# Performance work log

Measured on AMD Instinct MI355X. Metric: run time of the kernel, lower is better.

Reference implementation:

```python
import jax, jax.numpy as jnp
import numpy as np

HEADS = 16  # matches init_kwargs


def setup_inputs() -> dict:
    key = jax.random.key(0)
    ks = jax.random.split(key, 9)
    N, L, E, D = 2, 2048, 1024, 64
    return {
        "query": jax.random.normal(ks[0], (N, L, E), dtype=jnp.float32),
        "keys": jax.random.normal(ks[1], (N, L, E), dtype=jnp.float32),
        "values": jax.random.normal(ks[2], (N, L, E), dtype=jnp.float32),
        "masks": jax.random.randint(ks[3], (N, 1, 1, L), 0, 2, dtype=jnp.int32),
        "Wq": jax.random.normal(ks[4], (D, D), dtype=jnp.float32) / np.sqrt(D),
        "Wk": jax.random.normal(ks[5], (D, D), dtype=jnp.float32) / np.sqrt(D),
        "Wv": jax.random.normal(ks[6], (D, D), dtype=jnp.float32) / np.sqrt(D),
        "Wo": jax.random.normal(ks[7], (E, E), dtype=jnp.float32) / np.sqrt(E),
        "bo": jax.random.normal(ks[8], (E,), dtype=jnp.float32),
    }


def reference(query, keys, values, masks, Wq, Wk, Wv, Wo, bo):
    N, Lq, E = query.shape
    Lk = keys.shape[1]
    H = HEADS
    D = E // H
    # split heads: [N, L, H, D]
    q = query.reshape(N, Lq, H, D)
    k = keys.reshape(N, Lk, H, D)
    v = values.reshape(N, Lk, H, D)
    # per-head linear projections (weights shared across heads); Linear: x @ W.T
    q = jnp.einsum("nqhd,ed->nqhe", q, Wq)
    k = jnp.einsum("nkhd,ed->nkhe", k, Wk)
    v = jnp.einsum("nkhd,ed->nkhe", v, Wv)
    # scores [N, H, Lq, Lk]
    scores = jnp.einsum("nqhd,nkhd->nhqk", q, k)
    scores = jnp.where(masks == 0, jnp.float32(-1e20), scores)
    # NOTE: original scales by sqrt(embed_size), not sqrt(head_dim)
    attn = jax.nn.softmax(scores / jnp.sqrt(jnp.float32(E)), axis=3)
    out = jnp.einsum("nhqk,nkhd->nqhd", attn, v).reshape(N, Lq, E)
    return out @ Wo.T + bo
```

## Files before the change

kernel.cpp:

```cpp
#include <hip/hip_runtime.h>


typedef __bf16 bf16_t;
typedef __bf16 bf16x4 __attribute__((ext_vector_type(4)));
typedef __bf16 bf16x8 __attribute__((ext_vector_type(8)));
typedef float f32x4 __attribute__((ext_vector_type(4)));
typedef unsigned int u32x4 __attribute__((ext_vector_type(4)));

#define MFMA16(a, b, c) __builtin_amdgcn_mfma_f32_16x16x32_bf16((a), (b), (c), 0, 0, 0)

#define GLOAD_LDS16(gp, lp)                                              \
    __builtin_amdgcn_global_load_lds(                                    \
        (const __attribute__((address_space(1))) void*)(gp),             \
        (__attribute__((address_space(3))) void*)(lp), 16, 0, 0)

__device__ inline bf16x8 cvt8(const float* __restrict__ p) {
    f32x4 a = *(const f32x4*)p;
    f32x4 b = *(const f32x4*)(p + 4);
    bf16x8 r;
    r[0] = (bf16_t)a[0]; r[1] = (bf16_t)a[1];
    r[2] = (bf16_t)a[2]; r[3] = (bf16_t)a[3];
    r[4] = (bf16_t)b[0]; r[5] = (bf16_t)b[1];
    r[6] = (bf16_t)b[2]; r[7] = (bf16_t)b[3];
    return r;
}

__device__ inline bf16x8 cvt8s(const f32x4 a, const f32x4 b) {
    bf16x8 r;
    r[0] = (bf16_t)a[0]; r[1] = (bf16_t)a[1];
    r[2] = (bf16_t)a[2]; r[3] = (bf16_t)a[3];
    r[4] = (bf16_t)b[0]; r[5] = (bf16_t)b[1];
    r[6] = (bf16_t)b[2]; r[7] = (bf16_t)b[3];
    return r;
}

__device__ inline float exp2_fast(float x) {
    float r;
    asm("v_exp_f32 %0, %1" : "=v"(r) : "v"(x));
    return r;
}

__device__ inline unsigned cvt_pk_bf16(float lo, float hi) {
    unsigned r;
    asm("v_cvt_pk_bf16_f32 %0, %1, %2" : "=v"(r) : "v"(lo), "v"(hi));
    return r;
}

__device__ inline void xchg_quads(unsigned &x, unsigned &y) {
    asm("v_permlane32_swap_b32 %0, %1\n\t"
        "v_permlane16_swap_b32 %0, %1"
        : "+v"(x), "+v"(y));
}

__global__ __launch_bounds__(256) void scan_kernel(
    const int* __restrict__ msk, int* __restrict__ excl, int* __restrict__ lmap,
    const float* __restrict__ Wq, const float* __restrict__ Wk,
    const float* __restrict__ Wv,
    bf16_t* __restrict__ Wqb, bf16_t* __restrict__ Wkb, bf16_t* __restrict__ Wvb)
{
    const int t = threadIdx.x;

    if (blockIdx.x >= 2) {
        const int wi = blockIdx.x - 2;
        const float* Ws = (wi == 0) ? Wq : (wi == 1) ? Wk : Wv;
        bf16_t* Wb = (wi == 0) ? Wqb : (wi == 1) ? Wkb : Wvb;
        const float scale = (wi == 0) ? 0.04508422f : 1.0f;
        #pragma unroll
        for (int j = 0; j < 4; j++) {
            int idx = t * 16 + j * 4;
            f32x4 v = *(const f32x4*)&Ws[idx];
            bf16x4 r;
            r[0] = (bf16_t)(v[0] * scale); r[1] = (bf16_t)(v[1] * scale);
            r[2] = (bf16_t)(v[2] * scale); r[3] = (bf16_t)(v[3] * scale);
            *(bf16x4*)&Wb[idx] = r;
        }
        return;
    }

    __shared__ int wsum[4];
    const int n = blockIdx.x;
    const int lane = t & 63, w = t >> 6;
    const int* m = msk + n * 2048;
    int* e = excl + n * 2049;
    int* lm = lmap + n * 2048;

    int v[8], s = 0;
    #pragma unroll
    for (int j = 0; j < 8; j++) { v[j] = (m[t * 8 + j] != 0); s += v[j]; }

    int inc = s;
    #pragma unroll
    for (int d = 1; d < 64; d <<= 1) {
        int o = __shfl_up(inc, d);
        if (lane >= d) inc += o;
    }
    if (lane == 63) wsum[w] = inc;
    __syncthreads();
    int off = 0;
    #pragma unroll
    for (int i = 0; i < 4; i++)
        if (i < w) off += wsum[i];

    int a = off + inc - s;
    #pragma unroll
    for (int j = 0; j < 8; j++) {
        e[t * 8 + j] = a;
        if (v[j]) lm[a] = t * 8 + j;
        a += v[j];
    }
    if (t == 255) e[2048] = a;
}

__global__ __launch_bounds__(256) void qkv_proj_kernel(
    const float* __restrict__ kin, const float* __restrict__ vin,
    const bf16_t* __restrict__ Wkb, const bf16_t* __restrict__ Wvb,
    const float* __restrict__ Wo,
    const int* __restrict__ excl, const int* __restrict__ lmap,
    bf16_t* __restrict__ kc, bf16_t* __restrict__ vcT, bf16_t* __restrict__ Wob)
{
    __shared__ __align__(16) char smem[51200];

    const int t = threadIdx.x;
    const int w = t >> 6, lane = t & 63, quad = lane >> 4, l16 = lane & 15;

    if (blockIdx.y == 2) {
        int idx = blockIdx.x * 1024 + t * 4;
        f32x4 v = *(const f32x4*)&Wo[idx];
        bf16x4 r;
        r[0] = (bf16_t)v[0]; r[1] = (bf16_t)v[1];
        r[2] = (bf16_t)v[2]; r[3] = (bf16_t)v[3];
        *(bf16x4*)&Wob[idx] = r;
        return;
    }

    if (blockIdx.y == 1) {
        bf16_t* Ct = (bf16_t*)smem;
        const int h = blockIdx.x & 15;
        const int ctile = blockIdx.x >> 4;
        const int n = ctile >> 5;
        const int c0 = (ctile & 31) * 64;
        const int Lc = excl[n * 2049 + 2048];
        if (c0 >= Lc) return;

        const int p0 = w * 16 + l16;
        int cs = c0 + p0; if (cs > Lc - 1) cs = Lc - 1;
        const int tg = lmap[n * 2048 + cs];
        const size_t rb = ((size_t)(n * 2048 + tg)) * 1024 + h * 64;

        bf16x8 b0 = cvt8(&vin[rb + quad * 8]);
        bf16x8 b1 = cvt8(&vin[rb + 32 + quad * 8]);

        #pragma unroll
        for (int nt = 0; nt < 4; nt++) {
            bf16x8 a0 = *(const bf16x8*)&Wvb[(nt * 16 + l16) * 64 + quad * 8];
            bf16x8 a1 = *(const bf16x8*)&Wvb[(nt * 16 + l16) * 64 + 32 + quad * 8];
            f32x4 acc = {0.f, 0.f, 0.f, 0.f};
            acc = MFMA16(a0, b0, acc);
            acc = MFMA16(a1, b1, acc);
            #pragma unroll
            for (int r = 0; r < 4; r++)
                Ct[(nt * 16 + quad * 4 + r) * 72 + w * 16 + l16] = (bf16_t)acc[r];
        }
        __syncthreads();
        const int cnt = (Lc - c0 < 64) ? (Lc - c0) : 64;
        const size_t ob2 = ((size_t)(n * 16 + h)) * 131072 + c0;
        #pragma unroll
        for (int pass = 0; pass < 2; pass++) {
            int r = pass * 32 + (t >> 3);
            int cb8 = (t & 7) * 8;
            if (cb8 < cnt) {
                if (cb8 + 8 <= cnt) {
                    *(bf16x8*)&vcT[ob2 + (size_t)r * 2048 + cb8] =
                        *(const bf16x8*)&Ct[r * 72 + cb8];
                } else {
                    for (int q = cb8; q < cnt; q++)
                        vcT[ob2 + (size_t)r * 2048 + q] = Ct[r * 72 + q];
                }
            }
        }
        return;
    }

    if (blockIdx.x >= 512) return;
    const int n = blockIdx.x >> 8;
    const int c0 = (blockIdx.x & 255) * 8;
    const int Lc = excl[n * 2049 + 2048];
    if (c0 >= Lc) return;

    float* Xs = (float*)smem;
    bf16_t* Ct2 = (bf16_t*)(smem + 32768);

    #pragma unroll
    for (int j = 0; j < 8; j++) {
        int br = w * 32 + j * 4;
        int srow = br + (lane >> 4);
        int scol = ((lane & 15) ^ (srow & 15)) * 4;
        int csx = c0 + (srow >> 4); if (csx > Lc - 1) csx = Lc - 1;
        int hs = srow & 15;
        int ls = lmap[n * 2048 + csx];
        GLOAD_LDS16(&kin[((size_t)((n * 2048 + ls) * 16 + hs)) * 64 + scol], &Xs[br * 64]);
    }
    __syncthreads();

    const int rbase = w * 32;
    bf16x8 a[2][2];
    #pragma unroll
    for (int qs = 0; qs < 2; qs++) {
        int row = rbase + qs * 16 + l16;
        const char* rowp = (const char*)Xs + (size_t)row * 256;
        int swb = (row & 15) << 4;
        #pragma unroll
        for (int c = 0; c < 2; c++) {
            f32x4 lo = *(const f32x4*)(rowp + ((c * 128 + quad * 32) ^ swb));
            f32x4 hi = *(const f32x4*)(rowp + ((c * 128 + quad * 32 + 16) ^ swb));
            a[qs][c] = cvt8s(lo, hi);
        }
    }

    f32x4 acc[4][2];
    #pragma unroll
    for (int nt = 0; nt < 4; nt++) {
        bf16x8 b0 = *(const bf16x8*)&Wkb[(nt * 16 + l16) * 64 + quad * 8];
        bf16x8 b1 = *(const bf16x8*)&Wkb[(nt * 16 + l16) * 64 + 32 + quad * 8];
        #pragma unroll
        for (int qs = 0; qs < 2; qs++) {
            f32x4 z = {0.f, 0.f, 0.f, 0.f};
            z = MFMA16(a[qs][0], b0, z);
            z = MFMA16(a[qs][1], b1, z);
            acc[nt][qs] = z;
        }
    }

    #pragma unroll
    for (int nt = 0; nt < 4; nt++)
        #pragma unroll
        for (int qs = 0; qs < 2; qs++)
            #pragma unroll
            for (int r = 0; r < 4; r++)
                Ct2[(rbase + qs * 16 + quad * 4 + r) * 72 + nt * 16 + l16] = (bf16_t)acc[nt][qs][r];
    __syncthreads();

    #pragma unroll
    for (int it = 0; it < 4; it++) {
        int j = it * 32 + (t >> 3);
        bf16x8 val = *(const bf16x8*)&Ct2[j * 72 + (t & 7) * 8];
        int c = c0 + (j >> 4), h2 = j & 15;
        if (c < Lc)
            *(bf16x8*)&kc[(((size_t)(n * 16 + h2)) * 2048 + c) * 64 + (t & 7) * 8] = val;
    }
}

__global__ __launch_bounds__(256) void attn_kernel(
    const float* __restrict__ qin, const bf16_t* __restrict__ Wqb,
    const bf16_t* __restrict__ kc, const bf16_t* __restrict__ vcT,
    const int* __restrict__ excl, bf16_t* __restrict__ ao)
{
    __shared__ __align__(16) char smem[65536];
    bf16_t* KtP = (bf16_t*)smem;
    bf16_t* VtP = (bf16_t*)(smem + 32768);
#define KT(buf, r, c) KtP[(buf) * 8192 + (r) * 64 + (c)]
#define VT(buf, r, c) VtP[(buf) * 8192 + (r) * 128 + (c)]

    const int t = threadIdx.x;
    const int w = t >> 6, lane = t & 63, quad = lane >> 4, l16 = lane & 15;

    const int flat = blockIdx.x;
    const int xcd = flat & 7, slot = flat >> 3;
    const int nh = xcd * 4 + (slot >> 4), qb = slot & 15;
    const int n = nh >> 4, h = nh & 15;
    const int qbase = qb * 128 + w * 32;
    const size_t nhbase = (size_t)nh * 131072;

    const int Lc = excl[n * 2049 + 2048];
    const int ntiles = (Lc + 127) >> 7;
    const int rbase = w * 32;

    bf16x8 aq[2][2];
    {
        float* Xq = (float*)smem;
        bf16_t* Qt = (bf16_t*)(smem + 32768);
        const int qrow0 = qb * 128;
        #pragma unroll
        for (int j = 0; j < 8; j++) {
            int br = w * 32 + j * 4;
            int srow = br + (lane >> 4);
            int scol = ((lane & 15) ^ (srow & 15)) * 4;
            GLOAD_LDS16(&qin[((size_t)(n * 2048 + qrow0 + srow)) * 1024 + h * 64 + scol],
                        &Xq[br * 64]);
        }
        __syncthreads();

        bf16x8 a[2][2];
        #pragma unroll
        for (int qs = 0; qs < 2; qs++) {
            int row = rbase + qs * 16 + l16;
            const char* rowp = (const char*)Xq + (size_t)row * 256;
            int swb = (row & 15) << 4;
            #pragma unroll
            for (int c = 0; c < 2; c++) {
                f32x4 lo = *(const f32x4*)(rowp + ((c * 128 + quad * 32) ^ swb));
                f32x4 hi = *(const f32x4*)(rowp + ((c * 128 + quad * 32 + 16) ^ swb));
                a[qs][c] = cvt8s(lo, hi);
            }
        }
        f32x4 pacc[4][2];
        #pragma unroll
        for (int nt = 0; nt < 4; nt++) {
            bf16x8 b0 = *(const bf16x8*)&Wqb[(nt * 16 + l16) * 64 + quad * 8];
            bf16x8 b1 = *(const bf16x8*)&Wqb[(nt * 16 + l16) * 64 + 32 + quad * 8];
            #pragma unroll
            for (int qs = 0; qs < 2; qs++) {
                f32x4 z = {0.f, 0.f, 0.f, 0.f};
                z = MFMA16(a[qs][0], b0, z);
                z = MFMA16(a[qs][1], b1, z);
                pacc[nt][qs] = z;
            }
        }
        #pragma unroll
        for (int nt = 0; nt < 4; nt++)
            #pragma unroll
            for (int qs = 0; qs < 2; qs++)
                #pragma unroll
                for (int r = 0; r < 4; r++) {
                    int row = rbase + qs * 16 + quad * 4 + r;
                    int col = nt * 16 + l16;
                    int byteoff = row * 128 + ((((col >> 3) ^ (row & 7)) << 4) | ((col & 7) << 1));
                    *(bf16_t*)((char*)Qt + byteoff) = (bf16_t)pacc[nt][qs][r];
                }
        #pragma unroll
        for (int qs = 0; qs < 2; qs++) {
            int row = rbase + qs * 16 + l16;
            #pragma unroll
            for (int c = 0; c < 2; c++)
                aq[qs][c] = *(const bf16x8*)((const char*)Qt + row * 128 +
                                             (((c * 4 + quad) ^ (row & 7)) << 4));
        }
        __syncthreads();
    }

    f32x4 o[2][4];
    float lsum[2] = {0.f, 0.f};
    #pragma unroll
    for (int qs = 0; qs < 2; qs++)
        #pragma unroll
        for (int dt = 0; dt < 4; dt++) {
            o[qs][dt][0] = 0.f; o[qs][dt][1] = 0.f; o[qs][dt][2] = 0.f; o[qs][dt][3] = 0.f;
        }

    const int ksrow = lane >> 3;
    const int kscol = ((lane & 7) ^ (lane >> 3)) * 8;
    const int swr = l16 & 7;
    const int ck0 = (quad ^ swr) * 8;
    const int ck1 = ((quad + 4) ^ swr) * 8;

#define STAGE_KV(buf, kn)                                                     \
    {                                                                         \
        _Pragma("unroll")                                                     \
        for (int j = 0; j < 4; j++) {                                         \
            int rb = w * 32 + j * 8;                                          \
            GLOAD_LDS16(&kc[nhbase + (size_t)((kn) + rb + ksrow) * 64 + kscol],\
                        &KT(buf, rb, 0));                                     \
        }                                                                     \
        _Pragma("unroll")                                                     \
        for (int j = 0; j < 4; j++) {                                         \
            int rb = w * 16 + j * 4;                                          \
            int d = rb + (lane >> 4);                                         \
            int sc = ((lane & 15) ^ (d & 15)) * 8;                            \
            GLOAD_LDS16(&vcT[nhbase + (size_t)d * 2048 + (kn) + sc],          \
                        &VT(buf, rb, 0));                                     \
        }                                                                     \
    }

    STAGE_KV(0, 0);

    for (int i = 0; i < ntiles; i++) {
        const int cb = i & 1, nb = cb ^ 1;
        const int k0 = i * 128;
        __syncthreads();

        if (i + 1 < ntiles) STAGE_KV(nb, k0 + 128);

        #pragma unroll
        for (int hf = 0; hf < 2; hf++) {
            const int kh = k0 + hf * 64;

            f32x4 st[2][4];
            __builtin_amdgcn_s_setprio(1);
            #pragma unroll
            for (int ct = 0; ct < 4; ct++) {
                bf16x8 kb0 = *(const bf16x8*)&KT(cb, hf * 64 + ct * 16 + l16, ck0);
                bf16x8 kb1 = *(const bf16x8*)&KT(cb, hf * 64 + ct * 16 + l16, ck1);
                #pragma unroll
                for (int qs = 0; qs < 2; qs++) {
                    f32x4 acc = {0.f, 0.f, 0.f, 0.f};
                    acc = MFMA16(kb0, aq[qs][0], acc);
                    acc = MFMA16(kb1, aq[qs][1], acc);
                    st[qs][ct] = acc;
                }
            }
            __builtin_amdgcn_s_setprio(0);

            if (kh + 64 <= Lc) {
                #pragma unroll
                for (int qs = 0; qs < 2; qs++)
                    #pragma unroll
                    for (int ct = 0; ct < 4; ct++)
                        #pragma unroll
                        for (int r = 0; r < 4; r++) {
                            float p = exp2_fast(st[qs][ct][r]);
                            lsum[qs] += p;
                            st[qs][ct][r] = p;
                        }
            } else {
                #pragma unroll
                for (int qs = 0; qs < 2; qs++)
                    #pragma unroll
                    for (int ct = 0; ct < 4; ct++)
                        #pragma unroll
                        for (int r = 0; r < 4; r++) {
                            int kk = kh + ct * 16 + quad * 4 + r;
                            float p = (kk < Lc) ? exp2_fast(st[qs][ct][r]) : 0.0f;
                            lsum[qs] += p;
                            st[qs][ct][r] = p;
                        }
            }

            bf16x8 bp[2][2];
            #pragma unroll
            for (int qs = 0; qs < 2; qs++) {
                unsigned u[4][2];
                #pragma unroll
                for (int ct = 0; ct < 4; ct++) {
                    u[ct][0] = cvt_pk_bf16(st[qs][ct][0], st[qs][ct][1]);
                    u[ct][1] = cvt_pk_bf16(st[qs][ct][2], st[qs][ct][3]);
                }
                #pragma unroll
                for (int hh = 0; hh < 2; hh++) {
                    unsigned b0 = u[2 * hh][0], b2 = u[2 * hh + 1][0];
                    xchg_quads(b0, b2);
                    unsigned b1 = u[2 * hh][1], b3 = u[2 * hh + 1][1];
                    xchg_quads(b1, b3);
                    u32x4 q4 = {b0, b1, b2, b3};
                    bp[qs][hh] = __builtin_bit_cast(bf16x8, q4);
                }
            }

            __builtin_amdgcn_s_setprio(1);
            #pragma unroll
            for (int dt = 0; dt < 4; dt++) {
                bf16x8 va0 = *(const bf16x8*)&VT(cb, dt * 16 + l16, ((hf * 8 + quad) ^ l16) * 8);
                bf16x8 va1 = *(const bf16x8*)&VT(cb, dt * 16 + l16, ((hf * 8 + 4 + quad) ^ l16) * 8);
                #pragma unroll
                for (int qs = 0; qs < 2; qs++) {
                    o[qs][dt] = MFMA16(va0, bp[qs][0], o[qs][dt]);
                    o[qs][dt] = MFMA16(va1, bp[qs][1], o[qs][dt]);
                }
            }
            __builtin_amdgcn_s_setprio(0);
        }
    }

    #pragma unroll
    for (int qs = 0; qs < 2; qs++) {
        float v = lsum[qs];
        v += __shfl_xor(v, 16);
        v += __shfl_xor(v, 32);
        float inv = 1.0f / v;
        const int q = qb * 128 + w * 32 + qs * 16 + l16;
        const size_t base = ((size_t)n * 2048 + q) * 1024 + h * 64;
        #pragma unroll
        for (int dt = 0; dt < 4; dt++) {
            bf16x4 ov;
            #pragma unroll
            for (int r = 0; r < 4; r++) ov[r] = (bf16_t)(o[qs][dt][r] * inv);
            *(bf16x4*)&ao[base + dt * 16 + quad * 4] = ov;
        }
    }
#undef KT
#undef VT
#undef STAGE_KV
}

__global__ __launch_bounds__(256, 2) void out_proj_kernel(
    const bf16_t* __restrict__ X, const bf16_t* __restrict__ Wob,
    const float* __restrict__ bo, float* __restrict__ out)
{
    __shared__ bf16_t Xs[2][128][64];
    __shared__ bf16_t Ws[2][128][64];

    const int t = threadIdx.x;
    const int w = t >> 6, lane = t & 63, quad = lane >> 4, l16 = lane & 15;
    const int Mbase = blockIdx.x * 128;
    const int Nbase = blockIdx.y * 128;
    const int mrow = (w & 1) * 64;
    const int ncol = (w >> 1) * 64;

    const int scol = ((lane & 7) ^ (lane >> 3)) * 8;
    const int swr  = l16 & 7;

    f32x4 acc[4][4];
    #pragma unroll
    for (int mi = 0; mi < 4; mi++)
        #pragma unroll
        for (int ni = 0; ni < 4; ni++) {
            acc[mi][ni][0] = 0.f; acc[mi][ni][1] = 0.f;
            acc[mi][ni][2] = 0.f; acc[mi][ni][3] = 0.f;
        }

    #pragma unroll
    for (int j = 0; j < 4; j++) {
        int br = w * 32 + j * 8;
        GLOAD_LDS16(&X[(size_t)(Mbase + br + (lane >> 3)) * 1024 + scol], &Xs[0][br][0]);
        GLOAD_LDS16(&Wob[(size_t)(Nbase + br + (lane >> 3)) * 1024 + scol], &Ws[0][br][0]);
    }

    for (int i = 0; i < 16; i++) {
        const int cb = i & 1, nb = cb ^ 1;
        __syncthreads();

        if (i < 15) {
            const int kn = (i + 1) * 64;
            #pragma unroll
            for (int j = 0; j < 4; j++) {
                int br = w * 32 + j * 8;
                GLOAD_LDS16(&X[(size_t)(Mbase + br + (lane >> 3)) * 1024 + kn + scol],
                            &Xs[nb][br][0]);
                GLOAD_LDS16(&Wob[(size_t)(Nbase + br + (lane >> 3)) * 1024 + kn + scol],
                            &Ws[nb][br][0]);
            }
        }

        #pragma unroll
        for (int c = 0; c < 2; c++) {
            bf16x8 bfr[4];
            #pragma unroll
            for (int ni = 0; ni < 4; ni++)
                bfr[ni] = *(const bf16x8*)&Ws[cb][ncol + ni * 16 + l16][((c * 4 + quad) ^ swr) * 8];
            #pragma unroll
            for (int mi = 0; mi < 4; mi++) {
                bf16x8 afr = *(const bf16x8*)&Xs[cb][mrow + mi * 16 + l16][((c * 4 + quad) ^ swr) * 8];
                #pragma unroll
                for (int ni = 0; ni < 4; ni++)
                    acc[mi][ni] = MFMA16(afr, bfr[ni], acc[mi][ni]);
            }
        }
    }

    #pragma unroll
    for (int ni = 0; ni < 4; ni++) {
        float b = bo[Nbase + ncol + ni * 16 + l16];
        #pragma unroll
        for (int mi = 0; mi < 4; mi++) {
            #pragma unroll
            for (int r = 0; r < 4; r++) {
                int row = Mbase + mrow + mi * 16 + quad * 4 + r;
                out[(size_t)row * 1024 + Nbase + ncol + ni * 16 + l16] = acc[mi][ni][r] + b;
            }
        }
    }
}

extern "C" void kernel_launch(void* const* d_in, const int* in_sizes, int n_in,
                              void* d_out, int out_size, void* d_ws, size_t ws_size,
                              hipStream_t stream)
{
    const float* qin = (const float*)d_in[0];
    const float* kin = (const float*)d_in[1];
    const float* vin = (const float*)d_in[2];
    const int*   msk = (const int*)d_in[3];
    const float* Wq  = (const float*)d_in[4];
    const float* Wk  = (const float*)d_in[5];
    const float* Wv  = (const float*)d_in[6];
    const float* Wo  = (const float*)d_in[7];
    const float* bo  = (const float*)d_in[8];
    float* out = (float*)d_out;

    bf16_t* ws  = (bf16_t*)d_ws;
    bf16_t* kc  = ws + 4194304;
    bf16_t* vcT = ws + 8388608;
    bf16_t* ao  = ws + 12582912;
    bf16_t* Wob = ws + 16777216;
    int* excl   = (int*)(ws + 17825792);
    int* lmap   = excl + 4100;
    bf16_t* Wqb = (bf16_t*)(lmap + 4096);
    bf16_t* Wkb = Wqb + 4096;
    bf16_t* Wvb = Wkb + 4096;

    scan_kernel<<<5, 256, 0, stream>>>(msk, excl, lmap, Wq, Wk, Wv, Wqb, Wkb, Wvb);
    qkv_proj_kernel<<<dim3(1024, 3), 256, 0, stream>>>(kin, vin, Wkb, Wvb, Wo,
                                                        excl, lmap, kc, vcT, Wob);
    attn_kernel<<<dim3(512), 256, 0, stream>>>(qin, Wqb, kc, vcT, excl, ao);
    out_proj_kernel<<<dim3(32, 8), 256, 0, stream>>>(ao, Wob, bo, out);
}
```

Measured before the change: 158.4 us.

## Split attention block across eight waves with sixteen query rows each

The attention kernel now launches 512 threads per block, so each of eight waves handles 16 query rows instead of 32, and K/V staging is spread across more threads. This raises the wave count per CU to hide latency of LDS reads and exp work. In exchange, each wave reuses each K/V LDS fragment for fewer MFMAs, so LDS read traffic per unit of compute doubles, and the larger block may limit how many blocks fit per CU.

```diff
diff --git a/kernel.cpp b/kernel.cpp
--- a/kernel.cpp
+++ b/kernel.cpp
@@ -250,7 +250,7 @@
     }
 }
 
-__global__ __launch_bounds__(256) void attn_kernel(
+__global__ __launch_bounds__(512) void attn_kernel(
     const float* __restrict__ qin, const bf16_t* __restrict__ Wqb,
     const bf16_t* __restrict__ kc, const bf16_t* __restrict__ vcT,
     const int* __restrict__ excl, bf16_t* __restrict__ ao)
@@ -268,21 +268,20 @@
     const int xcd = flat & 7, slot = flat >> 3;
     const int nh = xcd * 4 + (slot >> 4), qb = slot & 15;
     const int n = nh >> 4, h = nh & 15;
-    const int qbase = qb * 128 + w * 32;
     const size_t nhbase = (size_t)nh * 131072;
 
     const int Lc = excl[n * 2049 + 2048];
     const int ntiles = (Lc + 127) >> 7;
-    const int rbase = w * 32;
-
-    bf16x8 aq[2][2];
+    const int rbase = w * 16;
+
+    bf16x8 aq[2];
     {
         float* Xq = (float*)smem;
         bf16_t* Qt = (bf16_t*)(smem + 32768);
         const int qrow0 = qb * 128;
         #pragma unroll
-        for (int j = 0; j < 8; j++) {
-            int br = w * 32 + j * 4;
+        for (int j = 0; j < 4; j++) {
+            int br = w * 16 + j * 4;
             int srow = br + (lane >> 4);
             int scol = ((lane & 15) ^ (srow & 15)) * 4;
             GLOAD_LDS16(&qin[((size_t)(n * 2048 + qrow0 + srow)) * 1024 + h * 64 + scol],
@@ -290,62 +289,53 @@
         }
         __syncthreads();
 
-        bf16x8 a[2][2];
-        #pragma unroll
-        for (int qs = 0; qs < 2; qs++) {
-            int row = rbase + qs * 16 + l16;
+        bf16x8 a[2];
+        {
+            int row = rbase + l16;
             const char* rowp = (const char*)Xq + (size_t)row * 256;
             int swb = (row & 15) << 4;
             #pragma unroll
             for (int c = 0; c < 2; c++) {
                 f32x4 lo = *(const f32x4*)(rowp + ((c * 128 + quad * 32) ^ swb));
                 f32x4 hi = *(const f32x4*)(rowp + ((c * 128 + quad * 32 + 16) ^ swb));
-                a[qs][c] = cvt8s(lo, hi);
-            }
-        }
-        f32x4 pacc[4][2];
+                a[c] = cvt8s(lo, hi);
+            }
+        }
+        f32x4 pacc[4];
         #pragma unroll
         for (int nt = 0; nt < 4; nt++) {
             bf16x8 b0 = *(const bf16x8*)&Wqb[(nt * 16 + l16) * 64 + quad * 8];
             bf16x8 b1 = *(const bf16x8*)&Wqb[(nt * 16 + l16) * 64 + 32 + quad * 8];
-            #pragma unroll
-            for (int qs = 0; qs < 2; qs++) {
-                f32x4 z = {0.f, 0.f, 0.f, 0.f};
-                z = MFMA16(a[qs][0], b0, z);
-                z = MFMA16(a[qs][1], b1, z);
-                pacc[nt][qs] = z;
-            }
+            f32x4 z = {0.f, 0.f, 0.f, 0.f};
+            z = MFMA16(a[0], b0, z);
+            z = MFMA16(a[1], b1, z);
+            pacc[nt] = z;
         }
         #pragma unroll
         for (int nt = 0; nt < 4; nt++)
             #pragma unroll
-            for (int qs = 0; qs < 2; qs++)
-                #pragma unroll
-                for (int r = 0; r < 4; r++) {
-                    int row = rbase + qs * 16 + quad * 4 + r;
-                    int col = nt * 16 + l16;
-                    int byteoff = row * 128 + ((((col >> 3) ^ (row & 7)) << 4) | ((col & 7) << 1));
-                    *(bf16_t*)((char*)Qt + byteoff) = (bf16_t)pacc[nt][qs][r];
-                }
-        #pragma unroll
-        for (int qs = 0; qs < 2; qs++) {
-            int row = rbase + qs * 16 + l16;
+            for (int r = 0; r < 4; r++) {
+                int row = rbase + quad * 4 + r;
+                int col = nt * 16 + l16;
+                int byteoff = row * 128 + ((((col >> 3) ^ (row & 7)) << 4) | ((col & 7) << 1));
+                *(bf16_t*)((char*)Qt + byteoff) = (bf16_t)pacc[nt][r];
+            }
+        {
+            int row = rbase + l16;
             #pragma unroll
             for (int c = 0; c < 2; c++)
-                aq[qs][c] = *(const bf16x8*)((const char*)Qt + row * 128 +
-                                             (((c * 4 + quad) ^ (row & 7)) << 4));
+                aq[c] = *(const bf16x8*)((const char*)Qt + row * 128 +
+                                         (((c * 4 + quad) ^ (row & 7)) << 4));
         }
         __syncthreads();
     }
 
-    f32x4 o[2][4];
-    float lsum[2] = {0.f, 0.f};
-    #pragma unroll
-    for (int qs = 0; qs < 2; qs++)
-        #pragma unroll
-        for (int dt = 0; dt < 4; dt++) {
-            o[qs][dt][0] = 0.f; o[qs][dt][1] = 0.f; o[qs][dt][2] = 0.f; o[qs][dt][3] = 0.f;
-        }
+    f32x4 o[4];
+    float lsum = 0.f;
+    #pragma unroll
+    for (int dt = 0; dt < 4; dt++) {
+        o[dt][0] = 0.f; o[dt][1] = 0.f; o[dt][2] = 0.f; o[dt][3] = 0.f;
+    }
 
     const int ksrow = lane >> 3;
     const int kscol = ((lane & 7) ^ (lane >> 3)) * 8;
@@ -356,14 +346,14 @@
 #define STAGE_KV(buf, kn)                                                     \
     {                                                                         \
         _Pragma("unroll")                                                     \
-        for (int j = 0; j < 4; j++) {                                         \
-            int rb = w * 32 + j * 8;                                          \
+        for (int j = 0; j < 2; j++) {                                         \
+            int rb = w * 16 + j * 8;                                          \
             GLOAD_LDS16(&kc[nhbase + (size_t)((kn) + rb + ksrow) * 64 + kscol],\
                         &KT(buf, rb, 0));                                     \
         }                                                                     \
         _Pragma("unroll")                                                     \
-        for (int j = 0; j < 4; j++) {                                         \
-            int rb = w * 16 + j * 4;                                          \
+        for (int j = 0; j < 2; j++) {                                         \
+            int rb = w * 8 + j * 4;                                           \
             int d = rb + (lane >> 4);                                         \
             int sc = ((lane & 15) ^ (d & 15)) * 8;                            \
             GLOAD_LDS16(&vcT[nhbase + (size_t)d * 2048 + (kn) + sc],          \
@@ -384,55 +374,47 @@
         for (int hf = 0; hf < 2; hf++) {
             const int kh = k0 + hf * 64;
 
-            f32x4 st[2][4];
+            f32x4 st[4];
             __builtin_amdgcn_s_setprio(1);
             #pragma unroll
             for (int ct = 0; ct < 4; ct++) {
                 bf16x8 kb0 = *(const bf16x8*)&KT(cb, hf * 64 + ct * 16 + l16, ck0);
                 bf16x8 kb1 = *(const bf16x8*)&KT(cb, hf * 64 + ct * 16 + l16, ck1);
-                #pragma unroll
-                for (int qs = 0; qs < 2; qs++) {
-                    f32x4 acc = {0.f, 0.f, 0.f, 0.f};
-                    acc = MFMA16(kb0, aq[qs][0], acc);
-                    acc = MFMA16(kb1, aq[qs][1], acc);
-                    st[qs][ct] = acc;
-                }
+                f32x4 acc = {0.f, 0.f, 0.f, 0.f};
+                acc = MFMA16(kb0, aq[0], acc);
+                acc = MFMA16(kb1, aq[1], acc);
+                st[ct] = acc;
             }
             __builtin_amdgcn_s_setprio(0);
 
             if (kh + 64 <= Lc) {
                 #pragma unroll
-                for (int qs = 0; qs < 2; qs++)
+                for (int ct = 0; ct < 4; ct++)
                     #pragma unroll
-                    for (int ct = 0; ct < 4; ct++)
-                        #pragma unroll
-                        for (int r = 0; r < 4; r++) {
-                            float p = exp2_fast(st[qs][ct][r]);
-                            lsum[qs] += p;
-                            st[qs][ct][r] = p;
-                        }
+                    for (int r = 0; r < 4; r++) {
+                        float p = exp2_fast(st[ct][r]);
+                        lsum += p;
+                        st[ct][r] = p;
+                    }
             } else {
                 #pragma unroll
-                for (int qs = 0; qs < 2; qs++)
+                for (int ct = 0; ct < 4; ct++)
                     #pragma unroll
-                    for (int ct = 0; ct < 4; ct++)
-                        #pragma unroll
-                        for (int r = 0; r < 4; r++) {
-                            int kk = kh + ct * 16 + quad * 4 + r;
-                            float p = (kk < Lc) ? exp2_fast(st[qs][ct][r]) : 0.0f;
-                            lsum[qs] += p;
-                            st[qs][ct][r] = p;
-                        }
-            }
-
-            bf16x8 bp[2][2];
-            #pragma unroll
-            for (int qs = 0; qs < 2; qs++) {
+                    for (int r = 0; r < 4; r++) {
+                        int kk = kh + ct * 16 + quad * 4 + r;
+                        float p = (kk < Lc) ? exp2_fast(st[ct][r]) : 0.0f;
+                        lsum += p;
+                        st[ct][r] = p;
+                    }
+            }
+
+            bf16x8 bp[2];
+            {
                 unsigned u[4][2];
                 #pragma unroll
                 for (int ct = 0; ct < 4; ct++) {
-                    u[ct][0] = cvt_pk_bf16(st[qs][ct][0], st[qs][ct][1]);
-                    u[ct][1] = cvt_pk_bf16(st[qs][ct][2], st[qs][ct][3]);
+                    u[ct][0] = cvt_pk_bf16(st[ct][0], st[ct][1]);
+                    u[ct][1] = cvt_pk_bf16(st[ct][2], st[ct][3]);
                 }
                 #pragma unroll
                 for (int hh = 0; hh < 2; hh++) {
@@ -441,7 +423,7 @@
                     unsigned b1 = u[2 * hh][1], b3 = u[2 * hh + 1][1];
                     xchg_quads(b1, b3);
                     u32x4 q4 = {b0, b1, b2, b3};
-                    bp[qs][hh] = __builtin_bit_cast(bf16x8, q4);
+                    bp[hh] = __builtin_bit_cast(bf16x8, q4);
                 }
             }
 
@@ -450,29 +432,25 @@
             for (int dt = 0; dt < 4; dt++) {
                 bf16x8 va0 = *(const bf16x8*)&VT(cb, dt * 16 + l16, ((hf * 8 + quad) ^ l16) * 8);
                 bf16x8 va1 = *(const bf16x8*)&VT(cb, dt * 16 + l16, ((hf * 8 + 4 + quad) ^ l16) * 8);
-                #pragma unroll
-                for (int qs = 0; qs < 2; qs++) {
-                    o[qs][dt] = MFMA16(va0, bp[qs][0], o[qs][dt]);
-                    o[qs][dt] = MFMA16(va1, bp[qs][1], o[qs][dt]);
-                }
+                o[dt] = MFMA16(va0, bp[0], o[dt]);
+                o[dt] = MFMA16(va1, bp[1], o[dt]);
             }
             __builtin_amdgcn_s_setprio(0);
         }
     }
 
-    #pragma unroll
-    for (int qs = 0; qs < 2; qs++) {
-        float v = lsum[qs];
+    {
+        float v = lsum;
         v += __shfl_xor(v, 16);
         v += __shfl_xor(v, 32);
         float inv = 1.0f / v;
-        const int q = qb * 128 + w * 32 + qs * 16 + l16;
+        const int q = qb * 128 + w * 16 + l16;
         const size_t base = ((size_t)n * 2048 + q) * 1024 + h * 64;
         #pragma unroll
         for (int dt = 0; dt < 4; dt++) {
             bf16x4 ov;
             #pragma unroll
-            for (int r = 0; r < 4; r++) ov[r] = (bf16_t)(o[qs][dt][r] * inv);
+            for (int r = 0; r < 4; r++) ov[r] = (bf16_t)(o[dt][r] * inv);
             *(bf16x4*)&ao[base + dt * 16 + quad * 4] = ov;
         }
     }
@@ -589,6 +567,6 @@
     scan_kernel<<<5, 256, 0, stream>>>(msk, excl, lmap, Wq, Wk, Wv, Wqb, Wkb, Wvb);
     qkv_proj_kernel<<<dim3(1024, 3), 256, 0, stream>>>(kin, vin, Wkb, Wvb, Wo,
                                                         excl, lmap, kc, vcT, Wob);
-    attn_kernel<<<dim3(512), 256, 0, stream>>>(qin, Wqb, kc, vcT, excl, ao);
+    attn_kernel<<<dim3(512), 512, 0, stream>>>(qin, Wqb, kc, vcT, excl, ao);
     out_proj_kernel<<<dim3(32, 8), 256, 0, stream>>>(ao, Wob, bo, out);
 }
```

Measured after the change: 156.2 us. About the same (-1.4%).

## Split attention over key range with combine kernel; shrink out-proj N tile

Applied to the files above, without the earlier changes.

Splits each (batch, head, query-block) attention work item into two halves of the compacted key range, doubling the attention grid to 1024 blocks. Each half writes unnormalized fp32 partial outputs and row sums, and a new combine kernel adds them and normalizes into bf16. The key tile shrinks to 64 with smaller LDS, and the output projection uses 64-wide N tiles to double its grid. This raises occupancy and fills more CUs, but adds an extra launch and an fp32 round trip through global memory.

```diff
diff --git a/kernel.cpp b/kernel.cpp
--- a/kernel.cpp
+++ b/kernel.cpp
@@ -253,32 +253,37 @@
 __global__ __launch_bounds__(256) void attn_kernel(
     const float* __restrict__ qin, const bf16_t* __restrict__ Wqb,
     const bf16_t* __restrict__ kc, const bf16_t* __restrict__ vcT,
-    const int* __restrict__ excl, bf16_t* __restrict__ ao)
+    const int* __restrict__ excl, float* __restrict__ po, float* __restrict__ ls)
 {
-    __shared__ __align__(16) char smem[65536];
+    __shared__ __align__(16) char smem[32768];
     bf16_t* KtP = (bf16_t*)smem;
-    bf16_t* VtP = (bf16_t*)(smem + 32768);
-#define KT(buf, r, c) KtP[(buf) * 8192 + (r) * 64 + (c)]
-#define VT(buf, r, c) VtP[(buf) * 8192 + (r) * 128 + (c)]
+    bf16_t* VtP = (bf16_t*)(smem + 16384);
+#define KT(buf, r, c) KtP[(buf) * 4096 + (r) * 64 + (c)]
+#define VT(buf, r, c) VtP[(buf) * 4096 + (r) * 64 + (c)]
 
     const int t = threadIdx.x;
     const int w = t >> 6, lane = t & 63, quad = lane >> 4, l16 = lane & 15;
 
     const int flat = blockIdx.x;
     const int xcd = flat & 7, slot = flat >> 3;
-    const int nh = xcd * 4 + (slot >> 4), qb = slot & 15;
+    const int nh = xcd * 4 + (slot >> 5);
+    const int qb = (slot >> 1) & 15;
+    const int s  = slot & 1;
     const int n = nh >> 4, h = nh & 15;
-    const int qbase = qb * 128 + w * 32;
     const size_t nhbase = (size_t)nh * 131072;
 
     const int Lc = excl[n * 2049 + 2048];
-    const int ntiles = (Lc + 127) >> 7;
+    const int ntot  = (Lc + 63) >> 6;
+    const int nhalf = (ntot + 1) >> 1;
+    const int tile0 = s ? nhalf : 0;
+    const int tile1 = s ? ntot : nhalf;
     const int rbase = w * 32;
+    const int qbase = qb * 128 + rbase;
 
     bf16x8 aq[2][2];
     {
         float* Xq = (float*)smem;
-        bf16_t* Qt = (bf16_t*)(smem + 32768);
+        bf16_t* Qt = (bf16_t*)(smem + 16384);
         const int qrow0 = qb * 128;
         #pragma unroll
         for (int j = 0; j < 8; j++) {
@@ -303,6 +308,8 @@
                 a[qs][c] = cvt8s(lo, hi);
             }
         }
+        __syncthreads();
+
         f32x4 pacc[4][2];
         #pragma unroll
         for (int nt = 0; nt < 4; nt++) {
@@ -327,6 +334,7 @@
                     int byteoff = row * 128 + ((((col >> 3) ^ (row & 7)) << 4) | ((col & 7) << 1));
                     *(bf16_t*)((char*)Qt + byteoff) = (bf16_t)pacc[nt][qs][r];
                 }
+        __syncthreads();
         #pragma unroll
         for (int qs = 0; qs < 2; qs++) {
             int row = rbase + qs * 16 + l16;
@@ -356,108 +364,97 @@
 #define STAGE_KV(buf, kn)                                                     \
     {                                                                         \
         _Pragma("unroll")                                                     \
-        for (int j = 0; j < 4; j++) {                                         \
-            int rb = w * 32 + j * 8;                                          \
+        for (int j = 0; j < 2; j++) {                                         \
+            int rb = w * 16 + j * 8;                                          \
             GLOAD_LDS16(&kc[nhbase + (size_t)((kn) + rb + ksrow) * 64 + kscol],\
                         &KT(buf, rb, 0));                                     \
-        }                                                                     \
-        _Pragma("unroll")                                                     \
-        for (int j = 0; j < 4; j++) {                                         \
-            int rb = w * 16 + j * 4;                                          \
-            int d = rb + (lane >> 4);                                         \
-            int sc = ((lane & 15) ^ (d & 15)) * 8;                            \
-            GLOAD_LDS16(&vcT[nhbase + (size_t)d * 2048 + (kn) + sc],          \
+            GLOAD_LDS16(&vcT[nhbase + (size_t)(rb + ksrow) * 2048 + (kn) + kscol],\
                         &VT(buf, rb, 0));                                     \
         }                                                                     \
     }
 
-    STAGE_KV(0, 0);
-
-    for (int i = 0; i < ntiles; i++) {
-        const int cb = i & 1, nb = cb ^ 1;
-        const int k0 = i * 128;
+    if (tile0 < tile1) STAGE_KV(0, tile0 * 64);
+
+    for (int i = tile0; i < tile1; i++) {
+        const int cb = (i - tile0) & 1, nb = cb ^ 1;
+        const int k0 = i * 64;
         __syncthreads();
 
-        if (i + 1 < ntiles) STAGE_KV(nb, k0 + 128);
-
-        #pragma unroll
-        for (int hf = 0; hf < 2; hf++) {
-            const int kh = k0 + hf * 64;
-
-            f32x4 st[2][4];
-            __builtin_amdgcn_s_setprio(1);
+        if (i + 1 < tile1) STAGE_KV(nb, k0 + 64);
+
+        f32x4 st[2][4];
+        __builtin_amdgcn_s_setprio(1);
+        #pragma unroll
+        for (int ct = 0; ct < 4; ct++) {
+            bf16x8 kb0 = *(const bf16x8*)&KT(cb, ct * 16 + l16, ck0);
+            bf16x8 kb1 = *(const bf16x8*)&KT(cb, ct * 16 + l16, ck1);
+            #pragma unroll
+            for (int qs = 0; qs < 2; qs++) {
+                f32x4 acc = {0.f, 0.f, 0.f, 0.f};
+                acc = MFMA16(kb0, aq[qs][0], acc);
+                acc = MFMA16(kb1, aq[qs][1], acc);
+                st[qs][ct] = acc;
+            }
+        }
+        __builtin_amdgcn_s_setprio(0);
+
+        if (k0 + 64 <= Lc) {
+            #pragma unroll
+            for (int qs = 0; qs < 2; qs++)
+                #pragma unroll
+                for (int ct = 0; ct < 4; ct++)
+                    #pragma unroll
+                    for (int r = 0; r < 4; r++) {
+                        float p = exp2_fast(st[qs][ct][r]);
+                        lsum[qs] += p;
+                        st[qs][ct][r] = p;
+                    }
+        } else {
+            #pragma unroll
+            for (int qs = 0; qs < 2; qs++)
+                #pragma unroll
+                for (int ct = 0; ct < 4; ct++)
+                    #pragma unroll
+                    for (int r = 0; r < 4; r++) {
+                        int kk = k0 + ct * 16 + quad * 4 + r;
+                        float p = (kk < Lc) ? exp2_fast(st[qs][ct][r]) : 0.0f;
+                        lsum[qs] += p;
+                        st[qs][ct][r] = p;
+                    }
+        }
+
+        bf16x8 bp[2][2];
+        #pragma unroll
+        for (int qs = 0; qs < 2; qs++) {
+            unsigned u[4][2];
             #pragma unroll
             for (int ct = 0; ct < 4; ct++) {
-                bf16x8 kb0 = *(const bf16x8*)&KT(cb, hf * 64 + ct * 16 + l16, ck0);
-                bf16x8 kb1 = *(const bf16x8*)&KT(cb, hf * 64 + ct * 16 + l16, ck1);
-                #pragma unroll
-                for (int qs = 0; qs < 2; qs++) {
-                    f32x4 acc = {0.f, 0.f, 0.f, 0.f};
-                    acc = MFMA16(kb0, aq[qs][0], acc);
-                    acc = MFMA16(kb1, aq[qs][1], acc);
-                    st[qs][ct] = acc;
-                }
-            }
-            __builtin_amdgcn_s_setprio(0);
-
-            if (kh + 64 <= Lc) {
-                #pragma unroll
-                for (int qs = 0; qs < 2; qs++)
-                    #pragma unroll
-                    for (int ct = 0; ct < 4; ct++)
-                        #pragma unroll
-                        for (int r = 0; r < 4; r++) {
-                            float p = exp2_fast(st[qs][ct][r]);
-                            lsum[qs] += p;
-                            st[qs][ct][r] = p;
-                        }
-            } else {
-                #pragma unroll
-                for (int qs = 0; qs < 2; qs++)
-                    #pragma unroll
-                    for (int ct = 0; ct < 4; ct++)
-                        #pragma unroll
-                        for (int r = 0; r < 4; r++) {
-                            int kk = kh + ct * 16 + quad * 4 + r;
-                            float p = (kk < Lc) ? exp2_fast(st[qs][ct][r]) : 0.0f;
-                            lsum[qs] += p;
-                            st[qs][ct][r] = p;
-                        }
-            }
-
-            bf16x8 bp[2][2];
+                u[ct][0] = cvt_pk_bf16(st[qs][ct][0], st[qs][ct][1]);
+                u[ct][1] = cvt_pk_bf16(st[qs][ct][2], st[qs][ct][3]);
+            }
+            #pragma unroll
+            for (int hh = 0; hh < 2; hh++) {
+                unsigned b0 = u[2 * hh][0], b2 = u[2 * hh + 1][0];
+                xchg_quads(b0, b2);
+                unsigned b1 = u[2 * hh][1], b3 = u[2 * hh + 1][1];
+                xchg_quads(b1, b3);
+                u32x4 q4 = {b0, b1, b2, b3};
+                bp[qs][hh] = __builtin_bit_cast(bf16x8, q4);
+            }
+        }
+
+        __builtin_amdgcn_s_setprio(1);
+        #pragma unroll
+        for (int dt = 0; dt < 4; dt++) {
+            bf16x8 va0 = *(const bf16x8*)&VT(cb, dt * 16 + l16, ck0);
+            bf16x8 va1 = *(const bf16x8*)&VT(cb, dt * 16 + l16, ck1);
             #pragma unroll
             for (int qs = 0; qs < 2; qs++) {
-                unsigned u[4][2];
-                #pragma unroll
-                for (int ct = 0; ct < 4; ct++) {
-                    u[ct][0] = cvt_pk_bf16(st[qs][ct][0], st[qs][ct][1]);
-                    u[ct][1] = cvt_pk_bf16(st[qs][ct][2], st[qs][ct][3]);
-                }
-                #pragma unroll
-                for (int hh = 0; hh < 2; hh++) {
-                    unsigned b0 = u[2 * hh][0], b2 = u[2 * hh + 1][0];
-                    xchg_quads(b0, b2);
-                    unsigned b1 = u[2 * hh][1], b3 = u[2 * hh + 1][1];
-                    xchg_quads(b1, b3);
-                    u32x4 q4 = {b0, b1, b2, b3};
-                    bp[qs][hh] = __builtin_bit_cast(bf16x8, q4);
-                }
-            }
-
-            __builtin_amdgcn_s_setprio(1);
-            #pragma unroll
-            for (int dt = 0; dt < 4; dt++) {
-                bf16x8 va0 = *(const bf16x8*)&VT(cb, dt * 16 + l16, ((hf * 8 + quad) ^ l16) * 8);
-                bf16x8 va1 = *(const bf16x8*)&VT(cb, dt * 16 + l16, ((hf * 8 + 4 + quad) ^ l16) * 8);
-                #pragma unroll
-                for (int qs = 0; qs < 2; qs++) {
-                    o[qs][dt] = MFMA16(va0, bp[qs][0], o[qs][dt]);
-                    o[qs][dt] = MFMA16(va1, bp[qs][1], o[qs][dt]);
-                }
-            }
-            __builtin_amdgcn_s_setprio(0);
-        }
+                o[qs][dt] = MFMA16(va0, bp[qs][0], o[qs][dt]);
+                o[qs][dt] = MFMA16(va1, bp[qs][1], o[qs][dt]);
+            }
+        }
+        __builtin_amdgcn_s_setprio(0);
     }
 
     #pragma unroll
@@ -465,20 +462,50 @@
         float v = lsum[qs];
         v += __shfl_xor(v, 16);
         v += __shfl_xor(v, 32);
-        float inv = 1.0f / v;
-        const int q = qb * 128 + w * 32 + qs * 16 + l16;
-        const size_t base = ((size_t)n * 2048 + q) * 1024 + h * 64;
-        #pragma unroll
-        for (int dt = 0; dt < 4; dt++) {
-            bf16x4 ov;
-            #pragma unroll
-            for (int r = 0; r < 4; r++) ov[r] = (bf16_t)(o[qs][dt][r] * inv);
-            *(bf16x4*)&ao[base + dt * 16 + quad * 4] = ov;
-        }
+        const int q = qbase + qs * 16 + l16;
+        const size_t pbase = ((size_t)(nh * 2 + s) * 2048 + q) * 64;
+        #pragma unroll
+        for (int dt = 0; dt < 4; dt++)
+            *(f32x4*)&po[pbase + dt * 16 + quad * 4] = o[qs][dt];
+        if (lane < 16) ls[(size_t)(nh * 2 + s) * 2048 + q] = v;
     }
 #undef KT
 #undef VT
 #undef STAGE_KV
+}
+
+__global__ __launch_bounds__(256) void combine_kernel(
+    const float* __restrict__ po, const float* __restrict__ ls,
+    bf16_t* __restrict__ ao)
+{
+    const int t = threadIdx.x;
+    const int nh = blockIdx.x >> 6;
+    const int qblk = blockIdx.x & 63;
+    const int n = nh >> 4, h = nh & 15;
+    const int q = qblk * 32 + (t >> 3);
+    const int dc = (t & 7) * 8;
+
+    float l0 = ls[(size_t)(nh * 2) * 2048 + q];
+    float l1 = ls[(size_t)(nh * 2 + 1) * 2048 + q];
+    float inv = 1.0f / (l0 + l1);
+
+    size_t b0 = ((size_t)(nh * 2) * 2048 + q) * 64 + dc;
+    size_t b1 = ((size_t)(nh * 2 + 1) * 2048 + q) * 64 + dc;
+    f32x4 a0 = *(const f32x4*)&po[b0];
+    f32x4 a1 = *(const f32x4*)&po[b0 + 4];
+    f32x4 c0 = *(const f32x4*)&po[b1];
+    f32x4 c1 = *(const f32x4*)&po[b1 + 4];
+
+    bf16x8 r;
+    r[0] = (bf16_t)((a0[0] + c0[0]) * inv);
+    r[1] = (bf16_t)((a0[1] + c0[1]) * inv);
+    r[2] = (bf16_t)((a0[2] + c0[2]) * inv);
+    r[3] = (bf16_t)((a0[3] + c0[3]) * inv);
+    r[4] = (bf16_t)((a1[0] + c1[0]) * inv);
+    r[5] = (bf16_t)((a1[1] + c1[1]) * inv);
+    r[6] = (bf16_t)((a1[2] + c1[2]) * inv);
+    r[7] = (bf16_t)((a1[3] + c1[3]) * inv);
+    *(bf16x8*)&ao[((size_t)n * 2048 + q) * 1024 + h * 64 + dc] = r;
 }
 
 __global__ __launch_bounds__(256, 2) void out_proj_kernel(
@@ -486,23 +513,23 @@
     const float* __restrict__ bo, float* __restrict__ out)
 {
     __shared__ bf16_t Xs[2][128][64];
-    __shared__ bf16_t Ws[2][128][64];
+    __shared__ bf16_t Ws[2][64][64];
 
     const int t = threadIdx.x;
     const int w = t >> 6, lane = t & 63, quad = lane >> 4, l16 = lane & 15;
     const int Mbase = blockIdx.x * 128;
-    const int Nbase = blockIdx.y * 128;
+    const int Nbase = blockIdx.y * 64;
     const int mrow = (w & 1) * 64;
-    const int ncol = (w >> 1) * 64;
+    const int ncol = (w >> 1) * 32;
 
     const int scol = ((lane & 7) ^ (lane >> 3)) * 8;
     const int swr  = l16 & 7;
 
-    f32x4 acc[4][4];
+    f32x4 acc[4][2];
     #pragma unroll
     for (int mi = 0; mi < 4; mi++)
         #pragma unroll
-        for (int ni = 0; ni < 4; ni++) {
+        for (int ni = 0; ni < 2; ni++) {
             acc[mi][ni][0] = 0.f; acc[mi][ni][1] = 0.f;
             acc[mi][ni][2] = 0.f; acc[mi][ni][3] = 0.f;
         }
@@ -511,6 +538,10 @@
     for (int j = 0; j < 4; j++) {
         int br = w * 32 + j * 8;
         GLOAD_LDS16(&X[(size_t)(Mbase + br + (lane >> 3)) * 1024 + scol], &Xs[0][br][0]);
+    }
+    #pragma unroll
+    for (int j = 0; j < 2; j++) {
+        int br = w * 16 + j * 8;
         GLOAD_LDS16(&Wob[(size_t)(Nbase + br + (lane >> 3)) * 1024 + scol], &Ws[0][br][0]);
     }
 
@@ -525,6 +556,10 @@
                 int br = w * 32 + j * 8;
                 GLOAD_LDS16(&X[(size_t)(Mbase + br + (lane >> 3)) * 1024 + kn + scol],
                             &Xs[nb][br][0]);
+            }
+            #pragma unroll
+            for (int j = 0; j < 2; j++) {
+                int br = w * 16 + j * 8;
                 GLOAD_LDS16(&Wob[(size_t)(Nbase + br + (lane >> 3)) * 1024 + kn + scol],
                             &Ws[nb][br][0]);
             }
@@ -532,22 +567,22 @@
 
         #pragma unroll
         for (int c = 0; c < 2; c++) {
-            bf16x8 bfr[4];
-            #pragma unroll
-            for (int ni = 0; ni < 4; ni++)
+            bf16x8 bfr[2];
+            #pragma unroll
+            for (int ni = 0; ni < 2; ni++)
                 bfr[ni] = *(const bf16x8*)&Ws[cb][ncol + ni * 16 + l16][((c * 4 + quad) ^ swr) * 8];
             #pragma unroll
             for (int mi = 0; mi < 4; mi++) {
                 bf16x8 afr = *(const bf16x8*)&Xs[cb][mrow + mi * 16 + l16][((c * 4 + quad) ^ swr) * 8];
                 #pragma unroll
-                for (int ni = 0; ni < 4; ni++)
+                for (int ni = 0; ni < 2; ni++)
                     acc[mi][ni] = MFMA16(afr, bfr[ni], acc[mi][ni]);
             }
         }
     }
 
     #pragma unroll
-    for (int ni = 0; ni < 4; ni++) {
+    for (int ni = 0; ni < 2; ni++) {
         float b = bo[Nbase + ncol + ni * 16 + l16];
         #pragma unroll
         for (int mi = 0; mi < 4; mi++) {
@@ -585,10 +620,13 @@
     bf16_t* Wqb = (bf16_t*)(lmap + 4096);
     bf16_t* Wkb = Wqb + 4096;
     bf16_t* Wvb = Wkb + 4096;
+    float* po   = (float*)((char*)d_ws + (40u << 20));
+    float* ls   = (float*)((char*)d_ws + (80u << 20));
 
     scan_kernel<<<5, 256, 0, stream>>>(msk, excl, lmap, Wq, Wk, Wv, Wqb, Wkb, Wvb);
     qkv_proj_kernel<<<dim3(1024, 3), 256, 0, stream>>>(kin, vin, Wkb, Wvb, Wo,
                                                         excl, lmap, kc, vcT, Wob);
-    attn_kernel<<<dim3(512), 256, 0, stream>>>(qin, Wqb, kc, vcT, excl, ao);
-    out_proj_kernel<<<dim3(32, 8), 256, 0, stream>>>(ao, Wob, bo, out);
-}
+    attn_kernel<<<dim3(1024), 256, 0, stream>>>(qin, Wqb, kc, vcT, excl, po, ls);
+    combine_kernel<<<dim3(2048), 256, 0, stream>>>(po, ls, ao);
+    out_proj_kernel<<<dim3(32, 16), 256, 0, stream>>>(ao, Wob, bo, out);
+}
```

New measurement: 170.1 us. +7.4%, slower.
